# Performance work log

Hardware: AMD Instinct MI355X
Metric: run time of the kernel (lower is better)

## Reference

```python
import jax, jax.numpy as jnp
import numpy as np

# dims: N = inner-loop slices (only last used), T = tensorLen, M = matrixSize, A = aux feat, D = dense units
N, T, M, A, D = 4, 1024, 128, 64, 128
RELU = True


def setup_inputs() -> dict:
    key = jax.random.key(0)
    k1, k2, k3, k4 = jax.random.split(key, 4)
    x_main = jax.random.normal(k1, (N, T, 1, M, M), dtype=jnp.float32)
    x_aux = jax.random.normal(k2, (M, T, A), dtype=jnp.float32)
    W1 = jax.random.normal(k3, (A, D), dtype=jnp.float32) * 0.05
    b1 = jnp.zeros((D,), dtype=jnp.float32)
    W2 = jax.random.normal(k4, (D, M), dtype=jnp.float32) * 0.05
    b2 = jnp.zeros((M,), dtype=jnp.float32)
    return {"x_main": x_main, "x_aux": x_aux, "W1": W1, "b1": b1, "W2": W2, "b2": b2}


def reference(x_main, x_aux, W1, b1, W2, b2):
    # SLAM sublayer applied to every aux slice at once: [M, T, A] -> [M, T, M]
    h = jnp.einsum('mta,ad->mtd', x_aux, W1) + b1
    if RELU:
        h = jax.nn.relu(h)
    S = jnp.einsum('mtd,dk->mtk', h, W2) + b2  # SLAM(aux_slice_t) stacked over t
    # Original inner loop overwrites outer_product -> only the LAST main slice matters.
    main_last = x_main[-1, :, 0]  # [T, M, M] (squeeze of [1, M, M])
    out = jnp.einsum('tij,jtk->tik', main_last, S)  # per-slice matmul, stacked: [T, M, M]
    # expand_dims(-1) then expand_dims(0): [1, T, M, M, 1]
    return out[None, :, :, :, None]
```

## Files before the change

### kernel.cpp

```cpp
#include <hip/hip_runtime.h>


#define TT 1024
#define MM 128
#define AA 64
#define DD 128

typedef float  f32x4  __attribute__((ext_vector_type(4)));
typedef __bf16 bf16x8 __attribute__((ext_vector_type(8)));
typedef __bf16 bf16x4 __attribute__((ext_vector_type(4)));


__global__ __launch_bounds__(512, 1)
void slam_fused(const float* __restrict__ xm, const float* __restrict__ xa,
                const float* __restrict__ W1, const float* __restrict__ b1,
                const float* __restrict__ W2, const float* __restrict__ b2,
                float* __restrict__ out)
{
    __shared__ __bf16 ldsR1[18432];
    __shared__ __bf16 ldsH [17408];
    __shared__ __bf16 ldsW2[17408];
    __shared__ float  ldsB1[128];
    __shared__ float  ldsB2[128];

    const int t    = blockIdx.x;
    const int tid  = threadIdx.x;
    const int lane = tid & 63;
    const int wv   = tid >> 6;
    const int n    = lane & 15;
    const int q    = lane >> 4;

    __bf16* Xal  = ldsR1;
    __bf16* W1Tl = ldsR1 + 9216;
    __bf16* Sl   = ldsR1;

    const float* arow = xm + (size_t)3 * TT * MM * MM + ((size_t)t * MM + wv * 16 + n) * MM;
    f32x4 apre[8];
#pragma unroll
    for (int ks = 0; ks < 4; ++ks) {
        apre[2 * ks]     = *(const f32x4*)(arow + ks * 32 + q * 8);
        apre[2 * ks + 1] = *(const f32x4*)(arow + ks * 32 + q * 8 + 4);
    }

#pragma unroll
    for (int p = 0; p < 4; ++p) {
        int m = p * 32 + (tid >> 4);
        int c = (tid & 15) * 4;
        f32x4 v = *(const f32x4*)(xa + ((size_t)m * TT + t) * AA + c);
        bf16x4 pk;
        pk[0] = (__bf16)v[0]; pk[1] = (__bf16)v[1]; pk[2] = (__bf16)v[2]; pk[3] = (__bf16)v[3];
        *(bf16x4*)(Xal + m * 72 + c) = pk;
    }
#pragma unroll
    for (int p = 0; p < 4; ++p) {
        int idx = p * 512 + tid;
        int a = idx >> 5;
        int d = (idx & 31) * 4;
        f32x4 v = *(const f32x4*)(W1 + a * DD + d);
        W1Tl[(d + 0) * 72 + a] = (__bf16)v[0];
        W1Tl[(d + 1) * 72 + a] = (__bf16)v[1];
        W1Tl[(d + 2) * 72 + a] = (__bf16)v[2];
        W1Tl[(d + 3) * 72 + a] = (__bf16)v[3];
    }
#pragma unroll
    for (int p = 0; p < 8; ++p) {
        int idx = p * 512 + tid;
        int d = idx >> 5;
        int k = (idx & 31) * 4;
        f32x4 v = *(const f32x4*)(W2 + d * DD + k);
        ldsW2[(k + 0) * 136 + d] = (__bf16)v[0];
        ldsW2[(k + 1) * 136 + d] = (__bf16)v[1];
        ldsW2[(k + 2) * 136 + d] = (__bf16)v[2];
        ldsW2[(k + 3) * 136 + d] = (__bf16)v[3];
    }
    if (tid < 128)      ldsB1[tid] = b1[tid];
    else if (tid < 256) ldsB2[tid - 128] = b2[tid - 128];

    __syncthreads();

    f32x4 acc[8];

    {
        bf16x8 a1[2];
#pragma unroll
        for (int ks = 0; ks < 2; ++ks)
            a1[ks] = *(const bf16x8*)(W1Tl + (wv * 16 + n) * 72 + ks * 32 + q * 8);
#pragma unroll
        for (int mt = 0; mt < 8; ++mt) acc[mt] = (f32x4){0.f, 0.f, 0.f, 0.f};
#pragma unroll
        for (int mt = 0; mt < 8; ++mt) {
#pragma unroll
            for (int ks = 0; ks < 2; ++ks) {
                bf16x8 bb = *(const bf16x8*)(Xal + (mt * 16 + n) * 72 + ks * 32 + q * 8);
                acc[mt] = __builtin_amdgcn_mfma_f32_16x16x32_bf16(a1[ks], bb, acc[mt], 0, 0, 0);
            }
        }
        int dbase = wv * 16 + q * 4;
        float bv0 = ldsB1[dbase + 0], bv1 = ldsB1[dbase + 1];
        float bv2 = ldsB1[dbase + 2], bv3 = ldsB1[dbase + 3];
#pragma unroll
        for (int mt = 0; mt < 8; ++mt) {
            int m = mt * 16 + n;
            bf16x4 pk;
            pk[0] = (__bf16)fmaxf(acc[mt][0] + bv0, 0.f);
            pk[1] = (__bf16)fmaxf(acc[mt][1] + bv1, 0.f);
            pk[2] = (__bf16)fmaxf(acc[mt][2] + bv2, 0.f);
            pk[3] = (__bf16)fmaxf(acc[mt][3] + bv3, 0.f);
            *(bf16x4*)(ldsH + m * 136 + dbase) = pk;
        }
    }
    __syncthreads();

    {
        bf16x8 a2[4];
#pragma unroll
        for (int ks = 0; ks < 4; ++ks)
            a2[ks] = *(const bf16x8*)(ldsH + (wv * 16 + n) * 136 + ks * 32 + q * 8);
#pragma unroll
        for (int kt = 0; kt < 8; ++kt) acc[kt] = (f32x4){0.f, 0.f, 0.f, 0.f};
#pragma unroll
        for (int kt = 0; kt < 8; ++kt) {
#pragma unroll
            for (int ks = 0; ks < 4; ++ks) {
                bf16x8 bb = *(const bf16x8*)(ldsW2 + (kt * 16 + n) * 136 + ks * 32 + q * 8);
                acc[kt] = __builtin_amdgcn_mfma_f32_16x16x32_bf16(a2[ks], bb, acc[kt], 0, 0, 0);
            }
        }
        int jbase = wv * 16 + q * 4;
#pragma unroll
        for (int kt = 0; kt < 8; ++kt) {
            int k = kt * 16 + n;
            float bv = ldsB2[k];
            bf16x4 pk;
            pk[0] = (__bf16)(acc[kt][0] + bv);
            pk[1] = (__bf16)(acc[kt][1] + bv);
            pk[2] = (__bf16)(acc[kt][2] + bv);
            pk[3] = (__bf16)(acc[kt][3] + bv);
            *(bf16x4*)(Sl + k * 136 + jbase) = pk;
        }
    }
    __syncthreads();

    {
        bf16x8 a3[4];
#pragma unroll
        for (int ks = 0; ks < 4; ++ks) {
            f32x4 lo = apre[2 * ks], hi = apre[2 * ks + 1];
            bf16x8 v;
            v[0] = (__bf16)lo[0]; v[1] = (__bf16)lo[1]; v[2] = (__bf16)lo[2]; v[3] = (__bf16)lo[3];
            v[4] = (__bf16)hi[0]; v[5] = (__bf16)hi[1]; v[6] = (__bf16)hi[2]; v[7] = (__bf16)hi[3];
            a3[ks] = v;
        }
#pragma unroll
        for (int kt = 0; kt < 8; ++kt) acc[kt] = (f32x4){0.f, 0.f, 0.f, 0.f};
#pragma unroll
        for (int kt = 0; kt < 8; ++kt) {
#pragma unroll
            for (int ks = 0; ks < 4; ++ks) {
                bf16x8 bb = *(const bf16x8*)(Sl + (kt * 16 + n) * 136 + ks * 32 + q * 8);
                acc[kt] = __builtin_amdgcn_mfma_f32_16x16x32_bf16(a3[ks], bb, acc[kt], 0, 0, 0);
            }
        }
        float* orow = out + (size_t)t * MM * MM;
        int ibase = wv * 16 + q * 4;
#pragma unroll
        for (int kt = 0; kt < 8; ++kt) {
            int k = kt * 16 + n;
#pragma unroll
            for (int r = 0; r < 4; ++r)
                orow[(size_t)(ibase + r) * MM + k] = acc[kt][r];
        }
    }
}

extern "C" void kernel_launch(void* const* d_in, const int* in_sizes, int n_in,
                              void* d_out, int out_size, void* d_ws, size_t ws_size,
                              hipStream_t stream) {
    const float* xm = (const float*)d_in[0];
    const float* xa = (const float*)d_in[1];
    const float* W1 = (const float*)d_in[2];
    const float* b1 = (const float*)d_in[3];
    const float* W2 = (const float*)d_in[4];
    const float* b2 = (const float*)d_in[5];
    float* out = (float*)d_out;
    slam_fused<<<dim3(TT), dim3(512), 0, stream>>>(xm, xa, W1, b1, W2, b2, out);
}
```

Measured before the change: 367.7 us.

## Process four time slices per block with register prefetch of next slice inputs

Each block now handles four consecutive t slices. Weights and biases are converted to bf16 in LDS once per block, and the next slice's x_main rows and x_aux tile are prefetched into registers while the current slice computes. LDS buffers are split so the input tile can be refilled without waiting on the S buffer. The weight transposes are rewritten so global reads are coalesced along the fast axis. The grid shrinks to a quarter, which reduces parallelism and relies on the in-block prefetch to hide memory latency.

```diff
diff --git a/kernel.cpp b/kernel.cpp
--- a/kernel.cpp
+++ b/kernel.cpp
@@ -5,6 +5,7 @@
 #define MM 128
 #define AA 64
 #define DD 128
+#define TPB 4
 
 typedef float  f32x4  __attribute__((ext_vector_type(4)));
 typedef __bf16 bf16x8 __attribute__((ext_vector_type(8)));
@@ -12,163 +13,198 @@
 
 
 __global__ __launch_bounds__(512, 1)
-void slam_fused(const float* __restrict__ xm, const float* __restrict__ xa,
-                const float* __restrict__ W1, const float* __restrict__ b1,
-                const float* __restrict__ W2, const float* __restrict__ b2,
-                float* __restrict__ out)
+void slam_fused2(const float* __restrict__ xm, const float* __restrict__ xa,
+                 const float* __restrict__ W1, const float* __restrict__ b1,
+                 const float* __restrict__ W2, const float* __restrict__ b2,
+                 float* __restrict__ out)
 {
-    __shared__ __bf16 ldsR1[18432];
-    __shared__ __bf16 ldsH [17408];
-    __shared__ __bf16 ldsW2[17408];
+    __shared__ __bf16 ldsW1T[ 9216];
+    __shared__ __bf16 ldsXa [ 9216];
+    __shared__ __bf16 ldsW2T[17408];
+    __shared__ __bf16 ldsH  [17408];
+    __shared__ __bf16 ldsS  [17408];
     __shared__ float  ldsB1[128];
     __shared__ float  ldsB2[128];
 
-    const int t    = blockIdx.x;
+    const int t0   = blockIdx.x * TPB;
     const int tid  = threadIdx.x;
     const int lane = tid & 63;
     const int wv   = tid >> 6;
     const int n    = lane & 15;
     const int q    = lane >> 4;
 
-    __bf16* Xal  = ldsR1;
-    __bf16* W1Tl = ldsR1 + 9216;
-    __bf16* Sl   = ldsR1;
-
-    const float* arow = xm + (size_t)3 * TT * MM * MM + ((size_t)t * MM + wv * 16 + n) * MM;
+    const float* abase = xm + (size_t)3 * TT * MM * MM;
     f32x4 apre[8];
-#pragma unroll
-    for (int ks = 0; ks < 4; ++ks) {
-        apre[2 * ks]     = *(const f32x4*)(arow + ks * 32 + q * 8);
-        apre[2 * ks + 1] = *(const f32x4*)(arow + ks * 32 + q * 8 + 4);
-    }
+    {
+        const float* arow = abase + ((size_t)t0 * MM + wv * 16 + n) * MM;
+#pragma unroll
+        for (int ks = 0; ks < 4; ++ks) {
+            apre[2 * ks]     = *(const f32x4*)(arow + ks * 32 + q * 8);
+            apre[2 * ks + 1] = *(const f32x4*)(arow + ks * 32 + q * 8 + 4);
+        }
+    }
+    const int xrow = tid >> 4;
+    const int xc   = (tid & 15) * 4;
+    f32x4 xpre[4];
+#pragma unroll
+    for (int p = 0; p < 4; ++p)
+        xpre[p] = *(const f32x4*)(xa + ((size_t)(p * 32 + xrow) * TT + t0) * AA + xc);
 
 #pragma unroll
     for (int p = 0; p < 4; ++p) {
-        int m = p * 32 + (tid >> 4);
-        int c = (tid & 15) * 4;
-        f32x4 v = *(const f32x4*)(xa + ((size_t)m * TT + t) * AA + c);
+        int ti = p * 512 + tid;
+        int d  = ti & 127;
+        int aq = ti >> 7;
         bf16x4 pk;
-        pk[0] = (__bf16)v[0]; pk[1] = (__bf16)v[1]; pk[2] = (__bf16)v[2]; pk[3] = (__bf16)v[3];
-        *(bf16x4*)(Xal + m * 72 + c) = pk;
-    }
-#pragma unroll
-    for (int p = 0; p < 4; ++p) {
-        int idx = p * 512 + tid;
-        int a = idx >> 5;
-        int d = (idx & 31) * 4;
-        f32x4 v = *(const f32x4*)(W1 + a * DD + d);
-        W1Tl[(d + 0) * 72 + a] = (__bf16)v[0];
-        W1Tl[(d + 1) * 72 + a] = (__bf16)v[1];
-        W1Tl[(d + 2) * 72 + a] = (__bf16)v[2];
-        W1Tl[(d + 3) * 72 + a] = (__bf16)v[3];
+#pragma unroll
+        for (int r = 0; r < 4; ++r)
+            pk[r] = (__bf16)W1[(size_t)(4 * aq + r) * DD + d];
+        *(bf16x4*)(ldsW1T + d * 72 + aq * 4) = pk;
     }
 #pragma unroll
     for (int p = 0; p < 8; ++p) {
-        int idx = p * 512 + tid;
-        int d = idx >> 5;
-        int k = (idx & 31) * 4;
-        f32x4 v = *(const f32x4*)(W2 + d * DD + k);
-        ldsW2[(k + 0) * 136 + d] = (__bf16)v[0];
-        ldsW2[(k + 1) * 136 + d] = (__bf16)v[1];
-        ldsW2[(k + 2) * 136 + d] = (__bf16)v[2];
-        ldsW2[(k + 3) * 136 + d] = (__bf16)v[3];
+        int ti = p * 512 + tid;
+        int k  = ti & 127;
+        int dq = ti >> 7;
+        bf16x4 pk;
+#pragma unroll
+        for (int r = 0; r < 4; ++r)
+            pk[r] = (__bf16)W2[(size_t)(4 * dq + r) * MM + k];
+        *(bf16x4*)(ldsW2T + k * 136 + dq * 4) = pk;
     }
     if (tid < 128)      ldsB1[tid] = b1[tid];
     else if (tid < 256) ldsB2[tid - 128] = b2[tid - 128];
 
+#pragma unroll
+    for (int p = 0; p < 4; ++p) {
+        bf16x4 pk;
+        pk[0] = (__bf16)xpre[p][0]; pk[1] = (__bf16)xpre[p][1];
+        pk[2] = (__bf16)xpre[p][2]; pk[3] = (__bf16)xpre[p][3];
+        *(bf16x4*)(ldsXa + (p * 32 + xrow) * 72 + xc) = pk;
+    }
+#pragma unroll
+    for (int p = 0; p < 4; ++p)
+        xpre[p] = *(const f32x4*)(xa + ((size_t)(p * 32 + xrow) * TT + (t0 + 1)) * AA + xc);
+
     __syncthreads();
 
     f32x4 acc[8];
-
-    {
-        bf16x8 a1[2];
-#pragma unroll
-        for (int ks = 0; ks < 2; ++ks)
-            a1[ks] = *(const bf16x8*)(W1Tl + (wv * 16 + n) * 72 + ks * 32 + q * 8);
-#pragma unroll
-        for (int mt = 0; mt < 8; ++mt) acc[mt] = (f32x4){0.f, 0.f, 0.f, 0.f};
-#pragma unroll
-        for (int mt = 0; mt < 8; ++mt) {
-#pragma unroll
-            for (int ks = 0; ks < 2; ++ks) {
-                bf16x8 bb = *(const bf16x8*)(Xal + (mt * 16 + n) * 72 + ks * 32 + q * 8);
-                acc[mt] = __builtin_amdgcn_mfma_f32_16x16x32_bf16(a1[ks], bb, acc[mt], 0, 0, 0);
-            }
-        }
-        int dbase = wv * 16 + q * 4;
-        float bv0 = ldsB1[dbase + 0], bv1 = ldsB1[dbase + 1];
-        float bv2 = ldsB1[dbase + 2], bv3 = ldsB1[dbase + 3];
-#pragma unroll
-        for (int mt = 0; mt < 8; ++mt) {
-            int m = mt * 16 + n;
-            bf16x4 pk;
-            pk[0] = (__bf16)fmaxf(acc[mt][0] + bv0, 0.f);
-            pk[1] = (__bf16)fmaxf(acc[mt][1] + bv1, 0.f);
-            pk[2] = (__bf16)fmaxf(acc[mt][2] + bv2, 0.f);
-            pk[3] = (__bf16)fmaxf(acc[mt][3] + bv3, 0.f);
-            *(bf16x4*)(ldsH + m * 136 + dbase) = pk;
-        }
-    }
-    __syncthreads();
-
-    {
-        bf16x8 a2[4];
-#pragma unroll
-        for (int ks = 0; ks < 4; ++ks)
-            a2[ks] = *(const bf16x8*)(ldsH + (wv * 16 + n) * 136 + ks * 32 + q * 8);
-#pragma unroll
-        for (int kt = 0; kt < 8; ++kt) acc[kt] = (f32x4){0.f, 0.f, 0.f, 0.f};
-#pragma unroll
-        for (int kt = 0; kt < 8; ++kt) {
+    for (int it = 0; it < TPB; ++it) {
+        const int t = t0 + it;
+
+        {
+            bf16x8 a1[2];
+#pragma unroll
+            for (int ks = 0; ks < 2; ++ks)
+                a1[ks] = *(const bf16x8*)(ldsW1T + (wv * 16 + n) * 72 + ks * 32 + q * 8);
+#pragma unroll
+            for (int mt = 0; mt < 8; ++mt) acc[mt] = (f32x4){0.f, 0.f, 0.f, 0.f};
+#pragma unroll
+            for (int mt = 0; mt < 8; ++mt) {
+#pragma unroll
+                for (int ks = 0; ks < 2; ++ks) {
+                    bf16x8 bb = *(const bf16x8*)(ldsXa + (mt * 16 + n) * 72 + ks * 32 + q * 8);
+                    acc[mt] = __builtin_amdgcn_mfma_f32_16x16x32_bf16(a1[ks], bb, acc[mt], 0, 0, 0);
+                }
+            }
+            int dbase = wv * 16 + q * 4;
+            float bv0 = ldsB1[dbase + 0], bv1 = ldsB1[dbase + 1];
+            float bv2 = ldsB1[dbase + 2], bv3 = ldsB1[dbase + 3];
+#pragma unroll
+            for (int mt = 0; mt < 8; ++mt) {
+                int m = mt * 16 + n;
+                bf16x4 pk;
+                pk[0] = (__bf16)fmaxf(acc[mt][0] + bv0, 0.f);
+                pk[1] = (__bf16)fmaxf(acc[mt][1] + bv1, 0.f);
+                pk[2] = (__bf16)fmaxf(acc[mt][2] + bv2, 0.f);
+                pk[3] = (__bf16)fmaxf(acc[mt][3] + bv3, 0.f);
+                *(bf16x4*)(ldsH + m * 136 + dbase) = pk;
+            }
+        }
+        __syncthreads();
+
+        if (it < TPB - 1) {
+#pragma unroll
+            for (int p = 0; p < 4; ++p) {
+                bf16x4 pk;
+                pk[0] = (__bf16)xpre[p][0]; pk[1] = (__bf16)xpre[p][1];
+                pk[2] = (__bf16)xpre[p][2]; pk[3] = (__bf16)xpre[p][3];
+                *(bf16x4*)(ldsXa + (p * 32 + xrow) * 72 + xc) = pk;
+            }
+        }
+
+        {
+            bf16x8 a2[4];
+#pragma unroll
+            for (int ks = 0; ks < 4; ++ks)
+                a2[ks] = *(const bf16x8*)(ldsH + (wv * 16 + n) * 136 + ks * 32 + q * 8);
+#pragma unroll
+            for (int kt = 0; kt < 8; ++kt) acc[kt] = (f32x4){0.f, 0.f, 0.f, 0.f};
+#pragma unroll
+            for (int kt = 0; kt < 8; ++kt) {
+#pragma unroll
+                for (int ks = 0; ks < 4; ++ks) {
+                    bf16x8 bb = *(const bf16x8*)(ldsW2T + (kt * 16 + n) * 136 + ks * 32 + q * 8);
+                    acc[kt] = __builtin_amdgcn_mfma_f32_16x16x32_bf16(a2[ks], bb, acc[kt], 0, 0, 0);
+                }
+            }
+            int jbase = wv * 16 + q * 4;
+#pragma unroll
+            for (int kt = 0; kt < 8; ++kt) {
+                int k = kt * 16 + n;
+                float bv = ldsB2[k];
+                bf16x4 pk;
+                pk[0] = (__bf16)(acc[kt][0] + bv);
+                pk[1] = (__bf16)(acc[kt][1] + bv);
+                pk[2] = (__bf16)(acc[kt][2] + bv);
+                pk[3] = (__bf16)(acc[kt][3] + bv);
+                *(bf16x4*)(ldsS + k * 136 + jbase) = pk;
+            }
+        }
+        __syncthreads();
+
+        {
+            bf16x8 a3[4];
 #pragma unroll
             for (int ks = 0; ks < 4; ++ks) {
-                bf16x8 bb = *(const bf16x8*)(ldsW2 + (kt * 16 + n) * 136 + ks * 32 + q * 8);
-                acc[kt] = __builtin_amdgcn_mfma_f32_16x16x32_bf16(a2[ks], bb, acc[kt], 0, 0, 0);
-            }
-        }
-        int jbase = wv * 16 + q * 4;
-#pragma unroll
-        for (int kt = 0; kt < 8; ++kt) {
-            int k = kt * 16 + n;
-            float bv = ldsB2[k];
-            bf16x4 pk;
-            pk[0] = (__bf16)(acc[kt][0] + bv);
-            pk[1] = (__bf16)(acc[kt][1] + bv);
-            pk[2] = (__bf16)(acc[kt][2] + bv);
-            pk[3] = (__bf16)(acc[kt][3] + bv);
-            *(bf16x4*)(Sl + k * 136 + jbase) = pk;
-        }
-    }
-    __syncthreads();
-
-    {
-        bf16x8 a3[4];
-#pragma unroll
-        for (int ks = 0; ks < 4; ++ks) {
-            f32x4 lo = apre[2 * ks], hi = apre[2 * ks + 1];
-            bf16x8 v;
-            v[0] = (__bf16)lo[0]; v[1] = (__bf16)lo[1]; v[2] = (__bf16)lo[2]; v[3] = (__bf16)lo[3];
-            v[4] = (__bf16)hi[0]; v[5] = (__bf16)hi[1]; v[6] = (__bf16)hi[2]; v[7] = (__bf16)hi[3];
-            a3[ks] = v;
-        }
-#pragma unroll
-        for (int kt = 0; kt < 8; ++kt) acc[kt] = (f32x4){0.f, 0.f, 0.f, 0.f};
-#pragma unroll
-        for (int kt = 0; kt < 8; ++kt) {
-#pragma unroll
-            for (int ks = 0; ks < 4; ++ks) {
-                bf16x8 bb = *(const bf16x8*)(Sl + (kt * 16 + n) * 136 + ks * 32 + q * 8);
-                acc[kt] = __builtin_amdgcn_mfma_f32_16x16x32_bf16(a3[ks], bb, acc[kt], 0, 0, 0);
-            }
-        }
-        float* orow = out + (size_t)t * MM * MM;
-        int ibase = wv * 16 + q * 4;
-#pragma unroll
-        for (int kt = 0; kt < 8; ++kt) {
-            int k = kt * 16 + n;
-#pragma unroll
-            for (int r = 0; r < 4; ++r)
-                orow[(size_t)(ibase + r) * MM + k] = acc[kt][r];
+                f32x4 lo = apre[2 * ks], hi = apre[2 * ks + 1];
+                bf16x8 v;
+                v[0] = (__bf16)lo[0]; v[1] = (__bf16)lo[1]; v[2] = (__bf16)lo[2]; v[3] = (__bf16)lo[3];
+                v[4] = (__bf16)hi[0]; v[5] = (__bf16)hi[1]; v[6] = (__bf16)hi[2]; v[7] = (__bf16)hi[3];
+                a3[ks] = v;
+            }
+            if (it < TPB - 1) {
+                const float* arow = abase + ((size_t)(t + 1) * MM + wv * 16 + n) * MM;
+#pragma unroll
+                for (int ks = 0; ks < 4; ++ks) {
+                    apre[2 * ks]     = *(const f32x4*)(arow + ks * 32 + q * 8);
+                    apre[2 * ks + 1] = *(const f32x4*)(arow + ks * 32 + q * 8 + 4);
+                }
+            }
+            if (it < TPB - 2) {
+#pragma unroll
+                for (int p = 0; p < 4; ++p)
+                    xpre[p] = *(const f32x4*)(xa + ((size_t)(p * 32 + xrow) * TT + (t + 2)) * AA + xc);
+            }
+#pragma unroll
+            for (int kt = 0; kt < 8; ++kt) acc[kt] = (f32x4){0.f, 0.f, 0.f, 0.f};
+#pragma unroll
+            for (int kt = 0; kt < 8; ++kt) {
+#pragma unroll
+                for (int ks = 0; ks < 4; ++ks) {
+                    bf16x8 bb = *(const bf16x8*)(ldsS + (kt * 16 + n) * 136 + ks * 32 + q * 8);
+                    acc[kt] = __builtin_amdgcn_mfma_f32_16x16x32_bf16(a3[ks], bb, acc[kt], 0, 0, 0);
+                }
+            }
+            float* orow = out + (size_t)t * MM * MM;
+            int ibase = wv * 16 + q * 4;
+#pragma unroll
+            for (int kt = 0; kt < 8; ++kt) {
+                int k = kt * 16 + n;
+#pragma unroll
+                for (int r = 0; r < 4; ++r)
+                    orow[(size_t)(ibase + r) * MM + k] = acc[kt][r];
+            }
         }
     }
 }
@@ -183,5 +219,5 @@
     const float* W2 = (const float*)d_in[4];
     const float* b2 = (const float*)d_in[5];
     float* out = (float*)d_out;
-    slam_fused<<<dim3(TT), dim3(512), 0, stream>>>(xm, xa, W1, b1, W2, b2, out);
+    slam_fused2<<<dim3(TT / TPB), dim3(512), 0, stream>>>(xm, xa, W1, b1, W2, b2, out);
 }
```

Result: no change. 360.9 us (-1.9%).
